# Kernel optimization log

Measured on AMD Instinct MI355X. Metric: run time of the kernel, lower is better.

Reference implementation:

```python
import jax, jax.numpy as jnp
import numpy as np

D_IN = 1024
D_OUT = 1024
SEQ = 4096


def setup_inputs() -> dict:
    key = jax.random.key(0)
    k0, k1, k2, k3 = jax.random.split(key, 4)
    inputs = jax.random.normal(k0, (SEQ, D_IN), dtype=jnp.float32)
    # original uses torch.rand (uniform [0,1)) for weights
    W_q = jax.random.uniform(k1, (D_IN, D_OUT), dtype=jnp.float32)
    W_k = jax.random.uniform(k2, (D_IN, D_OUT), dtype=jnp.float32)
    W_v = jax.random.uniform(k3, (D_IN, D_OUT), dtype=jnp.float32)
    return {"inputs": inputs, "W_q": W_q, "W_k": W_k, "W_v": W_v}


def reference(inputs, W_q, W_k, W_v):
    queries = inputs @ W_q            # [S, d_out]
    keys = inputs @ W_k               # [S, d_out]
    values = inputs @ W_v             # [S, d_out]
    d_k = keys.shape[-1]
    scale = 1.0 / jnp.sqrt(jnp.asarray(d_k, dtype=queries.dtype))
    attn_scores = queries @ keys.T    # [S, S]
    attn_weights = jax.nn.softmax(attn_scores * scale, axis=-1)
    context_vectors = attn_weights @ values  # [S, d_out]
    return context_vectors
```

## Files before the change

### kernel.cpp

```cpp
#include <hip/hip_runtime.h>

typedef unsigned short u16;
typedef __attribute__((ext_vector_type(8))) short bf16x8;
typedef __attribute__((ext_vector_type(4))) float f32x4;

#define SEQ 4096
#define DIM 1024

__device__ __forceinline__ u16 f2bf(float f) {
  unsigned u = __float_as_uint(f);
  return (u16)((u + 0x7fffu + ((u >> 16) & 1u)) >> 16);
}
__device__ __forceinline__ float bf2f(u16 h) {
  return __uint_as_float(((unsigned)h) << 16);
}

__device__ __forceinline__ void gload_lds16(const void* g, void* l) {
  __builtin_amdgcn_global_load_lds(
      (const __attribute__((address_space(1))) void*)g,
      (__attribute__((address_space(3))) void*)l, 16, 0, 0);
}

#define VM0 asm volatile("s_waitcnt vmcnt(0)" ::: "memory")
#define VM2 asm volatile("s_waitcnt vmcnt(2)" ::: "memory")
#define VM4 asm volatile("s_waitcnt vmcnt(4)" ::: "memory")
#define VM6 asm volatile("s_waitcnt vmcnt(6)" ::: "memory")
#define VM8 asm volatile("s_waitcnt vmcnt(8)" ::: "memory")
#define BAR __builtin_amdgcn_s_barrier()

__device__ __forceinline__ size_t pkoff(int row, int col, int kd) {
  int tile = (row >> 7) * (kd >> 5) + (col >> 5);
  int r7 = row & 127, c5 = col & 31;
  int slot = ((r7 >> 4) << 6) | ((c5 >> 3) << 4) | (r7 & 15);
  return (size_t)tile * 4096 + (size_t)(slot * 8 + (c5 & 7));
}

__device__ __forceinline__ void stage_tile_pk(const u16* __restrict__ g,
                                              u16* lds, int tid) {
  const int w = tid >> 6;
  gload_lds16(g + (size_t)tid * 8, lds + (size_t)(w * 64) * 8);
  gload_lds16(g + (size_t)(256 + tid) * 8, lds + (size_t)(256 + w * 64) * 8);
}

__device__ __forceinline__ void stage_q512(const u16* __restrict__ g,
                                           int kb, int nkb, u16* ldsq, int tid) {
  const int w = tid >> 6;
  gload_lds16(g + (size_t)kb * 4096 + tid * 8, ldsq + w * 512);
  gload_lds16(g + ((size_t)nkb + kb) * 4096 + tid * 8, ldsq + 4096 + w * 512);
}

__device__ __forceinline__ void gemm3_256(
    const u16* __restrict__ A0, const u16* __restrict__ A1,
    const u16* __restrict__ B0, const u16* __restrict__ B1,
    int nkb, u16* lds, f32x4 (&acc)[8][4]) {
  const int tid = threadIdx.x;
  const int w = tid >> 6, l = tid & 63;
  const int wm = w >> 2, wn = w & 3;

#pragma unroll
  for (int mi = 0; mi < 8; ++mi)
#pragma unroll
    for (int ni = 0; ni < 4; ++ni)
      acc[mi][ni] = (f32x4){0.f, 0.f, 0.f, 0.f};

  const int QA0 = 0, QA1 = 8192, QB0 = 16384, QB1 = 24576;
  const int aoff = wm * 4096 + l * 8;
  const int boff = ((wn & 2) >> 1) * 4096 + (wn & 1) * 2048 + l * 8;

  stage_q512(A0, 0, nkb, lds + QA0, tid);
  stage_q512(B0, 0, nkb, lds + QB0, tid);
  stage_q512(B1, 0, nkb, lds + QB1, tid);
  stage_q512(A1, 0, nkb, lds + QA1, tid);

  for (int kb = 0; kb < nkb; ++kb) {
    u16* cur = lds + (kb & 1) * 32768;
    u16* nxt = lds + ((kb + 1) & 1) * 32768;
    const bool pf = (kb + 1 < nkb);
    bf16x8 a0[8], b0[4];

    VM4;
    BAR;
    if (pf) {
      stage_q512(A0, kb + 1, nkb, nxt + QA0, tid);
      stage_q512(B0, kb + 1, nkb, nxt + QB0, tid);
    }
#pragma unroll
    for (int i = 0; i < 8; ++i) a0[i] = *(const bf16x8*)(cur + QA0 + aoff + i * 512);
#pragma unroll
    for (int i = 0; i < 4; ++i) b0[i] = *(const bf16x8*)(cur + QB0 + boff + i * 512);
    __builtin_amdgcn_s_setprio(1);
#pragma unroll
    for (int mi = 0; mi < 8; ++mi)
#pragma unroll
      for (int ni = 0; ni < 4; ++ni)
        acc[mi][ni] = __builtin_amdgcn_mfma_f32_16x16x32_bf16(
            a0[mi], b0[ni], acc[mi][ni], 0, 0, 0);
    __builtin_amdgcn_s_setprio(0);

    if (pf) { VM6; } else { VM2; }
    BAR;
    if (pf) stage_q512(B1, kb + 1, nkb, nxt + QB1, tid);
    {
      bf16x8 b1[4];
#pragma unroll
      for (int i = 0; i < 4; ++i) b1[i] = *(const bf16x8*)(cur + QB1 + boff + i * 512);
      __builtin_amdgcn_s_setprio(1);
#pragma unroll
      for (int mi = 0; mi < 8; ++mi)
#pragma unroll
        for (int ni = 0; ni < 4; ++ni)
          acc[mi][ni] = __builtin_amdgcn_mfma_f32_16x16x32_bf16(
              a0[mi], b1[ni], acc[mi][ni], 0, 0, 0);
      __builtin_amdgcn_s_setprio(0);
    }

    if (pf) { VM6; } else { VM0; }
    BAR;
    if (pf) stage_q512(A1, kb + 1, nkb, nxt + QA1, tid);
    {
      bf16x8 a1[8];
#pragma unroll
      for (int i = 0; i < 8; ++i) a1[i] = *(const bf16x8*)(cur + QA1 + aoff + i * 512);
      __builtin_amdgcn_s_setprio(1);
#pragma unroll
      for (int mi = 0; mi < 8; ++mi)
#pragma unroll
        for (int ni = 0; ni < 4; ++ni)
          acc[mi][ni] = __builtin_amdgcn_mfma_f32_16x16x32_bf16(
              a1[mi], b0[ni], acc[mi][ni], 0, 0, 0);
      __builtin_amdgcn_s_setprio(0);
    }
  }
  __syncthreads();
}

__device__ __forceinline__ void gemm1_256(
    const u16* __restrict__ A, const u16* __restrict__ B,
    int nkb, u16* lds, f32x4 (&acc)[8][4]) {
  const int tid = threadIdx.x;
  const int w = tid >> 6, l = tid & 63;
  const int wm = w >> 2, wn = w & 3;

#pragma unroll
  for (int mi = 0; mi < 8; ++mi)
#pragma unroll
    for (int ni = 0; ni < 4; ++ni)
      acc[mi][ni] = (f32x4){0.f, 0.f, 0.f, 0.f};

  const int aoff = wm * 4096 + l * 8;
  const int boff = ((wn & 2) >> 1) * 4096 + (wn & 1) * 2048 + l * 8;

  stage_q512(A, 0, nkb, lds + 0 * 16384, tid);
  stage_q512(B, 0, nkb, lds + 0 * 16384 + 8192, tid);
  stage_q512(A, 1, nkb, lds + 1 * 16384, tid);
  stage_q512(B, 1, nkb, lds + 1 * 16384 + 8192, tid);
  stage_q512(A, 2, nkb, lds + 2 * 16384, tid);
  stage_q512(B, 2, nkb, lds + 2 * 16384 + 8192, tid);

  for (int kb = 0; kb < nkb; ++kb) {
    if (kb + 2 < nkb) { VM8; } else if (kb + 1 < nkb) { VM4; } else { VM0; }
    BAR;
    if (kb + 3 < nkb) {
      u16* nb = lds + ((kb + 3) & 3) * 16384;
      stage_q512(A, kb + 3, nkb, nb, tid);
      stage_q512(B, kb + 3, nkb, nb + 8192, tid);
    }
    const u16* cb = lds + (kb & 3) * 16384;
    bf16x8 av[8], bv[4];
#pragma unroll
    for (int i = 0; i < 8; ++i) av[i] = *(const bf16x8*)(cb + aoff + i * 512);
#pragma unroll
    for (int i = 0; i < 4; ++i) bv[i] = *(const bf16x8*)(cb + 8192 + boff + i * 512);
    __builtin_amdgcn_s_setprio(1);
#pragma unroll
    for (int mi = 0; mi < 8; ++mi)
#pragma unroll
      for (int ni = 0; ni < 4; ++ni)
        acc[mi][ni] = __builtin_amdgcn_mfma_f32_16x16x32_bf16(
            av[mi], bv[ni], acc[mi][ni], 0, 0, 0);
    __builtin_amdgcn_s_setprio(0);
  }
  __syncthreads();
}

__device__ __forceinline__ void gemm1_db(
    const u16* A, const u16* B, int nkb, u16* lds, f32x4 (&acc)[4][4]) {
  const int tid = threadIdx.x;
  const int w = tid >> 6, l = tid & 63;
  const int wm = w >> 1, wn = w & 1;

#pragma unroll
  for (int mi = 0; mi < 4; ++mi)
#pragma unroll
    for (int ni = 0; ni < 4; ++ni)
      acc[mi][ni] = (f32x4){0.f, 0.f, 0.f, 0.f};

  const int ao = wm * 2048 + l * 8;
  const int bo = wn * 2048 + l * 8;
  const int nit = nkb >> 1;

  stage_tile_pk(A, lds, tid);
  stage_tile_pk(A + 4096, lds + 4096, tid);
  stage_tile_pk(B, lds + 8192, tid);
  stage_tile_pk(B + 4096, lds + 12288, tid);

  for (int it = 0; it < nit; ++it) {
    __syncthreads();
    if (it + 1 < nit) {
      u16* nb = lds + ((it + 1) & 1) * 16384;
      const size_t off = (size_t)(it + 1) * 8192;
      stage_tile_pk(A + off, nb, tid);
      stage_tile_pk(A + off + 4096, nb + 4096, tid);
      stage_tile_pk(B + off, nb + 8192, tid);
      stage_tile_pk(B + off + 4096, nb + 12288, tid);
    }
    const u16* cb = lds + (it & 1) * 16384;
#pragma unroll
    for (int ht = 0; ht < 2; ++ht) {
      bf16x8 av[4], bv[4];
#pragma unroll
      for (int i = 0; i < 4; ++i) {
        av[i] = *(const bf16x8*)(cb + ht * 4096 + ao + i * 512);
        bv[i] = *(const bf16x8*)(cb + 8192 + ht * 4096 + bo + i * 512);
      }
#pragma unroll
      for (int mi = 0; mi < 4; ++mi)
#pragma unroll
        for (int ni = 0; ni < 4; ++ni)
          acc[mi][ni] = __builtin_amdgcn_mfma_f32_16x16x32_bf16(
              av[mi], bv[ni], acc[mi][ni], 0, 0, 0);
    }
  }
  __syncthreads();
}

#define EPILOGUE_IDX                                          \
  const int tid = threadIdx.x, w = tid >> 6, l = tid & 63;    \
  const int wm = w >> 1, wn = w & 1, lr = l & 15, q = l >> 4; \
  (void)tid;

__device__ __forceinline__ void epilogue_pack256(
    f32x4 (&acc)[8][4], u16* lds, int row0, int col0, int kd,
    u16* __restrict__ H, u16* __restrict__ L) {
  const int tid = threadIdx.x, w = tid >> 6, l = tid & 63;
  const int wm = w >> 2, wn = w & 3, lr = l & 15, q = l >> 4;
  float* lC = (float*)lds;
#pragma unroll
  for (int p = 0; p < 4; ++p) {
    if (wm == (p >> 1)) {
      const int mib = (p & 1) * 4;
#pragma unroll
      for (int mi2 = 0; mi2 < 4; ++mi2)
#pragma unroll
        for (int ni = 0; ni < 4; ++ni)
#pragma unroll
          for (int r = 0; r < 4; ++r)
            lC[(mi2 * 16 + q * 4 + r) * 260 + wn * 64 + ni * 16 + lr] =
                acc[mib + mi2][ni][r];
    }
    __syncthreads();
#pragma unroll
    for (int j = 0; j < 2; ++j) {
      int u = tid + 512 * j;
      int row = u >> 4, c0 = (u & 15) * 16;
      u16 hbuf[16], lbuf[16];
#pragma unroll
      for (int i = 0; i < 16; ++i) {
        float v = lC[row * 260 + c0 + i];
        u16 hv = f2bf(v);
        hbuf[i] = hv;
        lbuf[i] = f2bf(v - bf2f(hv));
      }
      int rg = row0 + p * 64 + row;
      size_t o0 = pkoff(rg, col0 + c0, kd);
      size_t o1 = pkoff(rg, col0 + c0 + 8, kd);
      *(bf16x8*)(H + o0) = *(bf16x8*)(hbuf);
      *(bf16x8*)(H + o1) = *(bf16x8*)(hbuf + 8);
      if (L) {
        *(bf16x8*)(L + o0) = *(bf16x8*)(lbuf);
        *(bf16x8*)(L + o1) = *(bf16x8*)(lbuf + 8);
      }
    }
    if (p < 3) __syncthreads();
  }
}


__global__ __launch_bounds__(256) void prep_kernel(
    const float* __restrict__ X,
    const float* __restrict__ W0, const float* __restrict__ W1, const float* __restrict__ W2,
    u16* __restrict__ Xh, u16* __restrict__ Xl,
    u16* __restrict__ H0, u16* __restrict__ L0,
    u16* __restrict__ H1, u16* __restrict__ L1,
    u16* __restrict__ H2) {
  const int z = blockIdx.z;
  const int tx = threadIdx.x, ty = threadIdx.y;
  if (z == 0) {
    int idx = (blockIdx.y * 32 + blockIdx.x) * 256 + ty * 32 + tx;
    int row = idx >> 6;
    int c0 = (idx & 63) * 16;
    u16 h[16], lo[16];
#pragma unroll
    for (int j = 0; j < 4; ++j) {
      float4 x = *(const float4*)(X + (size_t)row * DIM + c0 + j * 4);
      float v;
      v = x.x; h[j*4+0] = f2bf(v); lo[j*4+0] = f2bf(v - bf2f(h[j*4+0]));
      v = x.y; h[j*4+1] = f2bf(v); lo[j*4+1] = f2bf(v - bf2f(h[j*4+1]));
      v = x.z; h[j*4+2] = f2bf(v); lo[j*4+2] = f2bf(v - bf2f(h[j*4+2]));
      v = x.w; h[j*4+3] = f2bf(v); lo[j*4+3] = f2bf(v - bf2f(h[j*4+3]));
    }
    size_t o0 = pkoff(row, c0, DIM);
    size_t o1 = pkoff(row, c0 + 8, DIM);
    *(bf16x8*)(Xh + o0) = *(bf16x8*)(h);
    *(bf16x8*)(Xl + o0) = *(bf16x8*)(lo);
    *(bf16x8*)(Xh + o1) = *(bf16x8*)(h + 8);
    *(bf16x8*)(Xl + o1) = *(bf16x8*)(lo + 8);
    return;
  }
  __shared__ float t[32][33];
  const float* W = (z == 1) ? W0 : (z == 2) ? W1 : W2;
  u16* H = (z == 1) ? H0 : (z == 2) ? H1 : H2;
  u16* L = (z == 1) ? L0 : (z == 2) ? L1 : nullptr;
  const int i0 = blockIdx.y * 32, o0 = blockIdx.x * 32;
#pragma unroll
  for (int m = 0; m < 4; ++m)
    t[ty + 8 * m][tx] = W[(size_t)(i0 + ty + 8 * m) * DIM + o0 + tx];
  __syncthreads();
#pragma unroll
  for (int m = 0; m < 4; ++m) {
    float v = t[tx][ty + 8 * m];
    u16 h = f2bf(v);
    size_t o = pkoff(o0 + ty + 8 * m, i0 + tx, DIM);
    H[o] = h;
    if (L) L[o] = f2bf(v - bf2f(h));
  }
}

__global__ __launch_bounds__(512, 2) void qkv_kernel(
    const u16* __restrict__ Xh, const u16* __restrict__ Xl,
    const u16* __restrict__ Wh0, const u16* __restrict__ Wl0,
    const u16* __restrict__ Wh1, const u16* __restrict__ Wl1,
    const u16* __restrict__ Wh2,
    u16* __restrict__ Qh, u16* __restrict__ Ql,
    u16* __restrict__ Kh, u16* __restrict__ Kl,
    u16* __restrict__ VT) {
  __shared__ __align__(16) u16 lds[2 * 32768];
  const int z = blockIdx.z;
  f32x4 acc[8][4];
  if (z < 2) {
    const u16* Wh = z ? Wh1 : Wh0;
    const u16* Wl = z ? Wl1 : Wl0;
    const int row0 = blockIdx.y * 256;
    const int col0 = blockIdx.x * 256;
    gemm3_256(Xh + (size_t)row0 * DIM, Xl + (size_t)row0 * DIM,
              Wh + (size_t)col0 * DIM, Wl + (size_t)col0 * DIM,
              DIM / 32, lds, acc);
    epilogue_pack256(acc, lds, row0, col0, DIM, z ? Kh : Qh, z ? Kl : Ql);
  } else {
    const int row0 = blockIdx.x * 256;
    const int col0 = blockIdx.y * 256;
    gemm1_256(Wh2 + (size_t)row0 * DIM, Xh + (size_t)col0 * DIM,
              DIM / 32, lds, acc);
    epilogue_pack256(acc, lds, row0, col0, SEQ, VT, nullptr);
  }
}

__global__ __launch_bounds__(512, 2) void s_kernel(
    const u16* __restrict__ Qh, const u16* __restrict__ Ql,
    const u16* __restrict__ Kh, const u16* __restrict__ Kl,
    float* __restrict__ S) {
  __shared__ __align__(16) u16 lds[2 * 32768];
  const int bid = blockIdx.y * 16 + blockIdx.x;
  const int xcd = bid & 7, c = bid >> 3;
  const int Y = (xcd & 3) * 4 + (c >> 3);
  const int X = (xcd >> 2) * 8 + (c & 7);
  const int row0 = Y * 256, col0 = X * 256;
  f32x4 acc[8][4];
  gemm3_256(Qh + (size_t)row0 * DIM, Ql + (size_t)row0 * DIM,
            Kh + (size_t)col0 * DIM, Kl + (size_t)col0 * DIM,
            DIM / 32, lds, acc);
  const int tid = threadIdx.x, w = tid >> 6, l = tid & 63;
  const int wm = w >> 2, wn = w & 3, lr = l & 15, q = l >> 4;
  const float scale = 0.03125f;
#pragma unroll
  for (int mi = 0; mi < 8; ++mi)
#pragma unroll
    for (int ni = 0; ni < 4; ++ni)
#pragma unroll
      for (int r = 0; r < 4; ++r) {
        int row = row0 + wm * 128 + mi * 16 + q * 4 + r;
        int col = col0 + wn * 64 + ni * 16 + lr;
        S[(size_t)row * SEQ + col] = acc[mi][ni][r] * scale;
      }
}

__global__ __launch_bounds__(256) void softmax_kernel(const float* __restrict__ S,
                                                      u16* __restrict__ P) {
  const int row = blockIdx.x;
  const float* s = S + (size_t)row * SEQ;
  const int tid = threadIdx.x;
  const int c0 = tid * 16;
  float v[16];
  float mx = -3.4e38f;
#pragma unroll
  for (int j = 0; j < 4; ++j) {
    float4 x = *(const float4*)(s + c0 + j * 4);
    v[j * 4 + 0] = x.x; v[j * 4 + 1] = x.y; v[j * 4 + 2] = x.z; v[j * 4 + 3] = x.w;
    mx = fmaxf(mx, fmaxf(fmaxf(x.x, x.y), fmaxf(x.z, x.w)));
  }
#pragma unroll
  for (int off = 32; off; off >>= 1) mx = fmaxf(mx, __shfl_xor(mx, off));
  __shared__ float red[8];
  const int w = tid >> 6, l = tid & 63;
  if (l == 0) red[w] = mx;
  __syncthreads();
  mx = fmaxf(fmaxf(red[0], red[1]), fmaxf(red[2], red[3]));
  float sum = 0.f;
#pragma unroll
  for (int i = 0; i < 16; ++i) {
    v[i] = __expf(v[i] - mx);
    sum += v[i];
  }
#pragma unroll
  for (int off = 32; off; off >>= 1) sum += __shfl_xor(sum, off);
  if (l == 0) red[4 + w] = sum;
  __syncthreads();
  sum = red[4] + red[5] + red[6] + red[7];
  const float inv = 1.f / sum;
  u16 p[16];
#pragma unroll
  for (int i = 0; i < 16; ++i) p[i] = f2bf(v[i] * inv);
  *(bf16x8*)(P + pkoff(row, c0, SEQ)) = *(bf16x8*)(p);
  *(bf16x8*)(P + pkoff(row, c0 + 8, SEQ)) = *(bf16x8*)(p + 8);
}

__global__ __launch_bounds__(256) void o_kernel(const u16* __restrict__ P,
                                                const u16* __restrict__ VT,
                                                float* __restrict__ Opart) {
  __shared__ __align__(16) u16 lds[2 * 4 * 4096];
  const int z = blockIdx.z;
  const int bid = blockIdx.y * 8 + blockIdx.x;
  const int xcd = bid & 7, c = bid >> 3;
  const int Y = xcd * 4 + (c >> 3);
  const int X = c & 7;
  const int row0 = Y * 128, col0 = X * 128;
  const u16* A = P + (size_t)row0 * SEQ + (size_t)z * 64 * 4096;
  const u16* B = VT + (size_t)col0 * SEQ + (size_t)z * 64 * 4096;
  f32x4 acc[4][4];
  gemm1_db(A, B, 64, lds, acc);
  EPILOGUE_IDX
  float* O = Opart + (size_t)z * SEQ * DIM;
#pragma unroll
  for (int mi = 0; mi < 4; ++mi)
#pragma unroll
    for (int ni = 0; ni < 4; ++ni)
#pragma unroll
      for (int r = 0; r < 4; ++r) {
        int row = row0 + wm * 64 + mi * 16 + q * 4 + r;
        int col = col0 + wn * 64 + ni * 16 + lr;
        O[(size_t)row * DIM + col] = acc[mi][ni][r];
      }
}

__global__ __launch_bounds__(256) void o_reduce_kernel(const float* __restrict__ Op,
                                                       float* __restrict__ O) {
  const size_t N = (size_t)SEQ * DIM;
  size_t i = ((size_t)blockIdx.x * 256 + threadIdx.x) * 4;
  float4 a = *(const float4*)(Op + i);
  float4 b = *(const float4*)(Op + N + i);
  float4 rr;
  rr.x = a.x + b.x;
  rr.y = a.y + b.y;
  rr.z = a.z + b.z;
  rr.w = a.w + b.w;
  *(float4*)(O + i) = rr;
}

extern "C" void kernel_launch(void* const* d_in, const int* in_sizes, int n_in,
                              void* d_out, int out_size, void* d_ws, size_t ws_size,
                              hipStream_t stream) {
  const float* X = (const float*)d_in[0];
  const float* Wq = (const float*)d_in[1];
  const float* Wk = (const float*)d_in[2];
  const float* Wv = (const float*)d_in[3];

  const size_t MB = 1024 * 1024;
  char* w = (char*)d_ws;
  u16* Xh = (u16*)(w + 0 * MB);
  u16* Xl = (u16*)(w + 8 * MB);
  u16* WqhT = (u16*)(w + 16 * MB);
  u16* WqlT = (u16*)(w + 18 * MB);
  u16* WkhT = (u16*)(w + 20 * MB);
  u16* WklT = (u16*)(w + 22 * MB);
  u16* WvhT = (u16*)(w + 24 * MB);
  u16* Qh = (u16*)(w + 26 * MB);
  u16* Ql = (u16*)(w + 34 * MB);
  u16* Kh = (u16*)(w + 42 * MB);
  u16* Kl = (u16*)(w + 50 * MB);
  u16* VT = (u16*)(w + 58 * MB);
  float* S = (float*)(w + 66 * MB);
  u16* P = (u16*)(w + 26 * MB);
  float* Opart = (float*)(w + 66 * MB);

  prep_kernel<<<dim3(32, 32, 4), dim3(32, 8), 0, stream>>>(
      X, Wq, Wk, Wv, Xh, Xl, WqhT, WqlT, WkhT, WklT, WvhT);
  qkv_kernel<<<dim3(DIM / 256, SEQ / 256, 3), 512, 0, stream>>>(
      Xh, Xl, WqhT, WqlT, WkhT, WklT, WvhT, Qh, Ql, Kh, Kl, VT);
  s_kernel<<<dim3(SEQ / 256, SEQ / 256), 512, 0, stream>>>(Qh, Ql, Kh, Kl, S);
  softmax_kernel<<<SEQ, 256, 0, stream>>>(S, P);
  o_kernel<<<dim3(DIM / 128, SEQ / 128, 2), 256, 0, stream>>>(P, VT, Opart);
  o_reduce_kernel<<<(SEQ * DIM) / (256 * 4), 256, 0, stream>>>(Opart, (float*)d_out);
}
```

Baseline: 308.4 us.

## Drop split-K in output GEMM and swizzle QKV block mapping across XCDs

The output GEMM no longer splits the K dimension into two halves with a separate reduction kernel. Each block now runs the full K loop and writes straight to the output, which removes the partial-buffer traffic and one launch but halves the grid to 256 blocks. The QKV kernel also remaps block indices so that blocks sharing row tiles land on the same XCD, aiming for better L2 reuse.

```diff
diff --git a/kernel.cpp b/kernel.cpp
--- a/kernel.cpp
+++ b/kernel.cpp
@@ -346,19 +346,23 @@
     u16* __restrict__ VT) {
   __shared__ __align__(16) u16 lds[2 * 32768];
   const int z = blockIdx.z;
+  const int bid = blockIdx.y * 4 + blockIdx.x;
+  const int xcd = bid & 7, c = bid >> 3;
+  const int Y = xcd * 2 + (c >> 2);
+  const int Xp = c & 3;
   f32x4 acc[8][4];
   if (z < 2) {
     const u16* Wh = z ? Wh1 : Wh0;
     const u16* Wl = z ? Wl1 : Wl0;
-    const int row0 = blockIdx.y * 256;
-    const int col0 = blockIdx.x * 256;
+    const int row0 = Y * 256;
+    const int col0 = Xp * 256;
     gemm3_256(Xh + (size_t)row0 * DIM, Xl + (size_t)row0 * DIM,
               Wh + (size_t)col0 * DIM, Wl + (size_t)col0 * DIM,
               DIM / 32, lds, acc);
     epilogue_pack256(acc, lds, row0, col0, DIM, z ? Kh : Qh, z ? Kl : Ql);
   } else {
-    const int row0 = blockIdx.x * 256;
-    const int col0 = blockIdx.y * 256;
+    const int row0 = Xp * 256;
+    const int col0 = Y * 256;
     gemm1_256(Wh2 + (size_t)row0 * DIM, Xh + (size_t)col0 * DIM,
               DIM / 32, lds, acc);
     epilogue_pack256(acc, lds, row0, col0, SEQ, VT, nullptr);
@@ -436,20 +440,18 @@
 
 __global__ __launch_bounds__(256) void o_kernel(const u16* __restrict__ P,
                                                 const u16* __restrict__ VT,
-                                                float* __restrict__ Opart) {
+                                                float* __restrict__ O) {
   __shared__ __align__(16) u16 lds[2 * 4 * 4096];
-  const int z = blockIdx.z;
   const int bid = blockIdx.y * 8 + blockIdx.x;
   const int xcd = bid & 7, c = bid >> 3;
   const int Y = xcd * 4 + (c >> 3);
   const int X = c & 7;
   const int row0 = Y * 128, col0 = X * 128;
-  const u16* A = P + (size_t)row0 * SEQ + (size_t)z * 64 * 4096;
-  const u16* B = VT + (size_t)col0 * SEQ + (size_t)z * 64 * 4096;
+  const u16* A = P + (size_t)row0 * SEQ;
+  const u16* B = VT + (size_t)col0 * SEQ;
   f32x4 acc[4][4];
-  gemm1_db(A, B, 64, lds, acc);
+  gemm1_db(A, B, 128, lds, acc);
   EPILOGUE_IDX
-  float* O = Opart + (size_t)z * SEQ * DIM;
 #pragma unroll
   for (int mi = 0; mi < 4; ++mi)
 #pragma unroll
@@ -460,20 +462,6 @@
         int col = col0 + wn * 64 + ni * 16 + lr;
         O[(size_t)row * DIM + col] = acc[mi][ni][r];
       }
-}
-
-__global__ __launch_bounds__(256) void o_reduce_kernel(const float* __restrict__ Op,
-                                                       float* __restrict__ O) {
-  const size_t N = (size_t)SEQ * DIM;
-  size_t i = ((size_t)blockIdx.x * 256 + threadIdx.x) * 4;
-  float4 a = *(const float4*)(Op + i);
-  float4 b = *(const float4*)(Op + N + i);
-  float4 rr;
-  rr.x = a.x + b.x;
-  rr.y = a.y + b.y;
-  rr.z = a.z + b.z;
-  rr.w = a.w + b.w;
-  *(float4*)(O + i) = rr;
 }
 
 extern "C" void kernel_launch(void* const* d_in, const int* in_sizes, int n_in,
@@ -500,7 +488,6 @@
   u16* VT = (u16*)(w + 58 * MB);
   float* S = (float*)(w + 66 * MB);
   u16* P = (u16*)(w + 26 * MB);
-  float* Opart = (float*)(w + 66 * MB);
 
   prep_kernel<<<dim3(32, 32, 4), dim3(32, 8), 0, stream>>>(
       X, Wq, Wk, Wv, Xh, Xl, WqhT, WqlT, WkhT, WklT, WvhT);
@@ -508,6 +495,5 @@
       Xh, Xl, WqhT, WqlT, WkhT, WklT, WvhT, Qh, Ql, Kh, Kl, VT);
   s_kernel<<<dim3(SEQ / 256, SEQ / 256), 512, 0, stream>>>(Qh, Ql, Kh, Kl, S);
   softmax_kernel<<<SEQ, 256, 0, stream>>>(S, P);
-  o_kernel<<<dim3(DIM / 128, SEQ / 128, 2), 256, 0, stream>>>(P, VT, Opart);
-  o_reduce_kernel<<<(SEQ * DIM) / (256 * 4), 256, 0, stream>>>(Opart, (float*)d_out);
-}
+  o_kernel<<<dim3(DIM / 128, SEQ / 128), 256, 0, stream>>>(P, VT, (float*)d_out);
+}
```

Result: no change. 310.4 us (+0.6%).
